# Optimization experiments

Measured on AMD Instinct MI355X. Metric: run time of the kernel, lower is better.

The kernel has to match this reference:

```python
import jax, jax.numpy as jnp
import numpy as np

B, T, D, U, R = 64, 512, 256, 256, 4


def setup_inputs() -> dict:
    key = jax.random.key(0)
    ks = jax.random.split(key, 12)
    inputs = jax.random.normal(ks[0], (B, T, D), dtype=jnp.float32)
    # per-timestep dependency indices into past timesteps; must satisfy dep[t] <= t
    dependencies = jnp.minimum(
        jax.random.randint(ks[1], (T, R - 1), 0, T), jnp.arange(T)[:, None]
    ).astype(jnp.int32)
    mask = jax.random.randint(ks[2], (B, T), 0, 2).astype(jnp.int32)
    initial_states = jax.random.normal(ks[3], (R, B, U), dtype=jnp.float32) * 0.1
    s = 1.0 / np.sqrt(U)
    def w(k, shape):
        return jax.random.normal(k, shape, dtype=jnp.float32) * s
    return dict(
        inputs=inputs, dependencies=dependencies, mask=mask, initial_states=initial_states,
        Wz=w(ks[4], (D, U)), Wr=w(ks[5], (D, U)), Wh=w(ks[6], (D, U)),
        Uz=w(ks[7], (U, U)), Ur=w(ks[8], (U, U)), Uh=w(ks[9], (U, U)),
        bz=jnp.zeros((U,), jnp.float32), br=jnp.zeros((U,), jnp.float32), bh=jnp.zeros((U,), jnp.float32),
    )


def reference(inputs, dependencies, mask, initial_states, Wz, Wr, Wh, Uz, Ur, Uh, bz, br, bh):
    Bn, Tn, _ = inputs.shape
    Rn = initial_states.shape[0]
    Un = Uz.shape[0]

    x = jnp.swapaxes(inputs, 0, 1)              # [T, B, D]  (time_major swap)
    m = jnp.swapaxes(mask, 0, 1).astype(bool)   # [T, B]
    # dependencies[i] is consumed AFTER step i (sets states for step i+1) -> shift by one
    dep_in = jnp.concatenate(
        [jnp.zeros((1, dependencies.shape[1]), dependencies.dtype), dependencies[:-1]], axis=0
    )

    def cell(x_t, states):
        # states: [R, B, U]  (child-sum Graph-GRU over recurrent_size predecessor states)
        r = jax.nn.sigmoid(x_t @ Wr + states @ Ur + br)          # [R, B, U]
        h_sum = states.sum(0)                                    # [B, U]
        z = jax.nn.sigmoid(x_t @ Wz + h_sum @ Uz + bz)
        h_tilde = jnp.tanh(x_t @ Wh + (r * states).sum(0) @ Uh + bh)
        h = z * (h_sum / Rn) + (1.0 - z) * h_tilde
        return h  # GRU: output == new state

    def step(carry, xs):
        prev_out, prev_state, buf, t = carry
        x_t, m_t, dep_t = xs
        gathered = buf[dep_t]                                    # [R-1, B, U] irregular history gather
        cand = jnp.concatenate([prev_state[None], gathered], axis=0)
        states = jnp.where(t == 0, initial_states, cand)
        h = cell(x_t, states)
        mt = m_t[:, None]                                        # [B, 1]
        out_m = jnp.where(mt, h, prev_out)                       # masked output (pre_output carry)
        st_m = jnp.where(mt, h, prev_state)                      # masked state  (pre_states carry)
        buf = buf.at[t].set(st_m)                                # successive_states[t]
        return (out_m, st_m, buf, t + 1), out_m

    carry0 = (
        jnp.zeros((Bn, Un), inputs.dtype),
        jnp.zeros((Bn, Un), inputs.dtype),
        jnp.zeros((Tn, Bn, Un), inputs.dtype),
        jnp.array(0, jnp.int32),
    )
    (last_out, last_state, _, _), outs = jax.lax.scan(step, carry0, (x, m, dep_in))

    # zero_output_for_mask
    last_out = jnp.where(m[-1][:, None], last_out, jnp.zeros_like(last_out))
    outs = jnp.where(m[:, :, None], outs, jnp.zeros_like(outs))
    outputs = jnp.swapaxes(outs, 0, 1)                           # back to [B, T, U]
    return outputs, last_out, last_state
```

## Files before the change

### kernel.cpp

```cpp
#include <hip/hip_runtime.h>
#include <cstdint>
#include <cstddef>

#define BN 64
#define TN 512
#define DN 256
#define UN 256
#define NC 768
#define SLOTS (TN + 5)
#define ZSLOT (TN + 4)

__device__ __forceinline__ float sigm(float x) {
  return 1.0f / (1.0f + __expf(-x));
}
__device__ __forceinline__ float tanh_fast(float x) {
  float e = __expf(-2.0f * x);
  return 2.0f / (1.0f + e) - 1.0f;
}

__global__ __launch_bounds__(256) void build_wcat(
    const float* __restrict__ Wr, const float* __restrict__ Wz, const float* __restrict__ Wh,
    const float* __restrict__ br, const float* __restrict__ bz, const float* __restrict__ bh,
    float* __restrict__ wcat, float* __restrict__ bias)
{
  int idx = blockIdx.x * 256 + threadIdx.x;
  if (idx < DN * NC) {
    int k = idx / NC, c = idx % NC;
    float v;
    if (c < 256)      v = Wr[k * UN + c];
    else if (c < 512) v = Wz[k * UN + (c - 256)];
    else              v = Wh[k * UN + (c - 512)];
    wcat[idx] = v;
  }
  if (idx < NC) {
    bias[idx] = (idx < 256) ? br[idx] : ((idx < 512) ? bz[idx - 256] : bh[idx - 512]);
  }
}

__global__ __launch_bounds__(256) void gemm_xw(
    const float* __restrict__ X, const float* __restrict__ Wc,
    const float* __restrict__ bias, float* __restrict__ P)
{
  __shared__ float As[32][68];
  __shared__ float Bs[32][64];
  const int tid = threadIdx.x;
  const int m0 = blockIdx.x * 64;
  const int n0 = blockIdx.y * 64;
  const int ty = tid >> 4, tx = tid & 15;
  float acc[4][4] = {};

  const int ar = tid >> 3;
  const int ak = (tid & 7) * 4;
  const int bk = tid >> 4;
  const int bn = (tid & 15) * 4;

  for (int k0 = 0; k0 < DN; k0 += 32) {
    float4 a0 = *(const float4*)(X + (size_t)(m0 + ar) * DN + k0 + ak);
    float4 a1 = *(const float4*)(X + (size_t)(m0 + 32 + ar) * DN + k0 + ak);
    As[ak + 0][ar] = a0.x; As[ak + 1][ar] = a0.y; As[ak + 2][ar] = a0.z; As[ak + 3][ar] = a0.w;
    As[ak + 0][32 + ar] = a1.x; As[ak + 1][32 + ar] = a1.y; As[ak + 2][32 + ar] = a1.z; As[ak + 3][32 + ar] = a1.w;
    *(float4*)&Bs[bk][bn]      = *(const float4*)(Wc + (size_t)(k0 + bk) * NC + n0 + bn);
    *(float4*)&Bs[bk + 16][bn] = *(const float4*)(Wc + (size_t)(k0 + bk + 16) * NC + n0 + bn);
    __syncthreads();
#pragma unroll
    for (int kk = 0; kk < 32; kk++) {
      float4 av = *(const float4*)&As[kk][ty * 4];
      float4 bv = *(const float4*)&Bs[kk][tx * 4];
      acc[0][0] += av.x * bv.x; acc[0][1] += av.x * bv.y; acc[0][2] += av.x * bv.z; acc[0][3] += av.x * bv.w;
      acc[1][0] += av.y * bv.x; acc[1][1] += av.y * bv.y; acc[1][2] += av.y * bv.z; acc[1][3] += av.y * bv.w;
      acc[2][0] += av.z * bv.x; acc[2][1] += av.z * bv.y; acc[2][2] += av.z * bv.z; acc[2][3] += av.z * bv.w;
      acc[3][0] += av.w * bv.x; acc[3][1] += av.w * bv.y; acc[3][2] += av.w * bv.z; acc[3][3] += av.w * bv.w;
    }
    __syncthreads();
  }
  float4 bb = *(const float4*)(bias + n0 + tx * 4);
#pragma unroll
  for (int i = 0; i < 4; i++) {
    float4 o;
    o.x = acc[i][0] + bb.x; o.y = acc[i][1] + bb.y;
    o.z = acc[i][2] + bb.z; o.w = acc[i][3] + bb.w;
    *(float4*)(P + (size_t)(m0 + ty * 4 + i) * NC + n0 + tx * 4) = o;
  }
}

__global__ __launch_bounds__(1024, 4) void recurrent_kernel(
    const float* __restrict__ P,
    const float* __restrict__ Ur, const float* __restrict__ Uz, const float* __restrict__ Uh,
    const int* __restrict__ dep, const int* __restrict__ mask,
    const float* __restrict__ init,
    float* __restrict__ out,
    float* __restrict__ buf_s, float* __restrict__ buf_pr, float* __restrict__ buf_pz)
{
  const int b = blockIdx.x;
  const int tid = threadIdx.x;
  const int g = tid >> 8;
  const int u = tid & 255;
  const int qd = tid >> 6;
  const int cd = (tid & 63) * 4;

  float wh[64];
  {
    const float* p2 = Uh + (size_t)(64 * g) * UN + u;
#pragma unroll
    for (int kk = 0; kk < 64; kk++) {
      wh[kk] = p2[(size_t)kk * UN];
    }
  }

  __shared__ float ls[4][256], lpr[4][256], lpz[4][256];
  __shared__ float lx[NC];
  __shared__ float rs[256], hs[256], zv[256], hv[256];
  __shared__ float red0[4][256];
  __shared__ float reddR[16][256], reddZ[16][256];
  __shared__ float scur[256], prcur[256], pzcur[256];
  __shared__ int eff[TN];
  __shared__ int mloc[TN];
  __shared__ int deploc[TN * 3];

  for (int i = tid; i < TN; i += 1024) mloc[i] = mask[b * TN + i];
  for (int i = tid; i < TN * 3; i += 1024) deploc[i] = dep[i];

  const size_t bufBase = (size_t)b * SLOTS * UN;

  {
    float v = init[((size_t)g * BN + b) * UN + u];
    ls[g][u] = v;
    buf_s[bufBase + (size_t)(TN + g) * UN + u] = v;
    if (tid < 256) {
      scur[u] = 0.0f; prcur[u] = 0.0f; pzcur[u] = 0.0f;
      buf_s[bufBase + (size_t)ZSLOT * UN + u] = 0.0f;
      buf_pr[bufBase + (size_t)ZSLOT * UN + u] = 0.0f;
      buf_pz[bufBase + (size_t)ZSLOT * UN + u] = 0.0f;
    }
  }
  __syncthreads();

#pragma unroll 1
  for (int gg = 0; gg < 4; gg++) {
    float4 arA = {0, 0, 0, 0}, azA = {0, 0, 0, 0};
    const float* bR = Ur + (size_t)(qd * 16) * UN + cd;
    const float* bZ = Uz + (size_t)(qd * 16) * UN + cd;
#pragma unroll 4
    for (int kk = 0; kk < 16; kk++) {
      float hk = ls[gg][qd * 16 + kk];
      float4 w1 = *(const float4*)(bR + (size_t)kk * UN);
      float4 w2 = *(const float4*)(bZ + (size_t)kk * UN);
      arA.x = fmaf(hk, w1.x, arA.x); arA.y = fmaf(hk, w1.y, arA.y);
      arA.z = fmaf(hk, w1.z, arA.z); arA.w = fmaf(hk, w1.w, arA.w);
      azA.x = fmaf(hk, w2.x, azA.x); azA.y = fmaf(hk, w2.y, azA.y);
      azA.z = fmaf(hk, w2.z, azA.z); azA.w = fmaf(hk, w2.w, azA.w);
    }
    *(float4*)&reddR[qd][cd] = arA;
    *(float4*)&reddZ[qd][cd] = azA;
    __syncthreads();
    if (tid < 256) {
      float prn = 0.0f, pzn = 0.0f;
#pragma unroll
      for (int q = 0; q < 16; q++) { prn += reddR[q][tid]; pzn += reddZ[q][tid]; }
      buf_pr[bufBase + (size_t)(TN + gg) * UN + tid] = prn;
      buf_pz[bufBase + (size_t)(TN + gg) * UN + tid] = pzn;
    }
    __syncthreads();
  }

  const size_t outB = (size_t)b * TN * UN;
  const size_t pB = (size_t)b * TN * NC;

#pragma unroll 1
  for (int t = 0; t < TN; t++) {
    const int m = mloc[t];
    if (m == 0) {
      if (tid < 256) out[outB + (size_t)t * UN + u] = 0.0f;
      if (tid == 0) eff[t] = (t == 0) ? ZSLOT : eff[t - 1];
      __syncthreads();
      continue;
    }
    if (t > 0 && g == 0) {
      ls[0][u] = scur[u]; lpr[0][u] = prcur[u]; lpz[0][u] = pzcur[u];
    } else {
      int src = (t == 0) ? (TN + g) : eff[deploc[(t - 1) * 3 + (g - 1)]];
      size_t base = bufBase + (size_t)src * UN + u;
      ls[g][u]  = buf_s[base];
      lpr[g][u] = buf_pr[base];
      lpz[g][u] = buf_pz[base];
    }
    if (tid < NC) lx[tid] = P[pB + (size_t)t * NC + tid];
    __syncthreads();
    if (tid < 256) {
      float s0 = ls[0][u], s1 = ls[1][u], s2 = ls[2][u], s3 = ls[3][u];
      float xr = lx[u];
      float r0 = sigm(xr + lpr[0][u]);
      float r1 = sigm(xr + lpr[1][u]);
      float r2 = sigm(xr + lpr[2][u]);
      float r3 = sigm(xr + lpr[3][u]);
      rs[u] = r0 * s0 + r1 * s1 + r2 * s2 + r3 * s3;
      hs[u] = (s0 + s1) + (s2 + s3);
      zv[u] = sigm(lx[256 + u] + ((lpz[0][u] + lpz[1][u]) + (lpz[2][u] + lpz[3][u])));
    }
    __syncthreads();
    {
      float a0 = 0, a1 = 0, a2 = 0, a3 = 0;
      const float4* v4 = (const float4*)&rs[64 * g];
#pragma unroll
      for (int kk = 0; kk < 16; kk++) {
        float4 v = v4[kk];
        a0 += v.x * wh[4 * kk];     a1 += v.y * wh[4 * kk + 1];
        a2 += v.z * wh[4 * kk + 2]; a3 += v.w * wh[4 * kk + 3];
      }
      red0[g][u] = (a0 + a1) + (a2 + a3);
    }
    __syncthreads();
    if (tid < 256) {
      float ht = tanh_fast(lx[512 + u] + ((red0[0][u] + red0[1][u]) + (red0[2][u] + red0[3][u])));
      float z = zv[u];
      float h = z * hs[u] * 0.25f + (1.0f - z) * ht;
      hv[u] = h; scur[u] = h;
      out[outB + (size_t)t * UN + u] = h;
    }
    __syncthreads();
    {
      float4 arA = {0, 0, 0, 0}, azA = {0, 0, 0, 0};
      const float* bR = Ur + (size_t)(qd * 16) * UN + cd;
      const float* bZ = Uz + (size_t)(qd * 16) * UN + cd;
#pragma unroll 4
      for (int kk = 0; kk < 16; kk++) {
        float hk = hv[qd * 16 + kk];
        float4 w1 = *(const float4*)(bR + (size_t)kk * UN);
        float4 w2 = *(const float4*)(bZ + (size_t)kk * UN);
        arA.x = fmaf(hk, w1.x, arA.x); arA.y = fmaf(hk, w1.y, arA.y);
        arA.z = fmaf(hk, w1.z, arA.z); arA.w = fmaf(hk, w1.w, arA.w);
        azA.x = fmaf(hk, w2.x, azA.x); azA.y = fmaf(hk, w2.y, azA.y);
        azA.z = fmaf(hk, w2.z, azA.z); azA.w = fmaf(hk, w2.w, azA.w);
      }
      *(float4*)&reddR[qd][cd] = arA;
      *(float4*)&reddZ[qd][cd] = azA;
    }
    __syncthreads();
    if (tid < 256) {
      float prn = 0.0f, pzn = 0.0f;
#pragma unroll
      for (int q = 0; q < 16; q++) { prn += reddR[q][tid]; pzn += reddZ[q][tid]; }
      prcur[tid] = prn; pzcur[tid] = pzn;
      size_t base = bufBase + (size_t)t * UN + tid;
      buf_s[base]  = hv[tid];
      buf_pr[base] = prn;
      buf_pz[base] = pzn;
    }
    if (tid == 0) eff[t] = t;
    __syncthreads();
  }

  if (tid < 256) {
    float lst = scur[u];
    out[(size_t)BN * TN * UN + (size_t)b * UN + u] = mloc[TN - 1] ? lst : 0.0f;
    out[(size_t)BN * TN * UN + (size_t)BN * UN + (size_t)b * UN + u] = lst;
  }
}

extern "C" void kernel_launch(void* const* d_in, const int* in_sizes, int n_in,
                              void* d_out, int out_size, void* d_ws, size_t ws_size,
                              hipStream_t stream) {
  const float* inputs       = (const float*)d_in[0];
  const int*   dependencies = (const int*)d_in[1];
  const int*   mask         = (const int*)d_in[2];
  const float* initial      = (const float*)d_in[3];
  const float* Wz = (const float*)d_in[4];
  const float* Wr = (const float*)d_in[5];
  const float* Wh = (const float*)d_in[6];
  const float* Uz = (const float*)d_in[7];
  const float* Ur = (const float*)d_in[8];
  const float* Uh = (const float*)d_in[9];
  const float* bz = (const float*)d_in[10];
  const float* br = (const float*)d_in[11];
  const float* bh = (const float*)d_in[12];

  float* out = (float*)d_out;
  float* ws  = (float*)d_ws;
  float* wcat    = ws;
  float* bias    = wcat + (size_t)DN * NC;
  float* precomp = bias + NC;
  float* buf_s   = precomp + (size_t)BN * TN * NC;
  float* buf_pr  = buf_s + (size_t)BN * SLOTS * UN;
  float* buf_pz  = buf_pr + (size_t)BN * SLOTS * UN;

  build_wcat<<<(DN * NC + 255) / 256, 256, 0, stream>>>(Wr, Wz, Wh, br, bz, bh, wcat, bias);
  gemm_xw<<<dim3(BN * TN / 64, NC / 64), 256, 0, stream>>>(inputs, wcat, bias, precomp);
  recurrent_kernel<<<BN, 1024, 0, stream>>>(precomp, Ur, Uz, Uh, dependencies, mask, initial,
                                            out, buf_s, buf_pr, buf_pz);
}
```

Baseline: 2.062 ms.

## Cache leading rows of Ur/Uz in LDS and split projection by matrix

Restructures the per-step Ur/Uz projection so each wave handles a single matrix over a 32-row k-slice, instead of both matrices over a 16-row slice. The first WL=6 rows of each slice are preloaded into shared memory and the remaining rows still stream from global/L2. The partial-sum reduction drops from 16 to 8 terms per output. This cuts global weight traffic on the serial critical path, at the cost of about 96KB more LDS per block and a longer per-wave k-loop.

After: 1.870 ms. 1.1x faster.

```diff
diff --git a/kernel.cpp b/kernel.cpp
--- a/kernel.cpp
+++ b/kernel.cpp
@@ -9,6 +9,7 @@
 #define NC 768
 #define SLOTS (TN + 5)
 #define ZSLOT (TN + 4)
+#define WL 6
 
 __device__ __forceinline__ float sigm(float x) {
   return 1.0f / (1.0f + __expf(-x));
@@ -95,8 +96,10 @@
   const int tid = threadIdx.x;
   const int g = tid >> 8;
   const int u = tid & 255;
-  const int qd = tid >> 6;
-  const int cd = (tid & 63) * 4;
+  const int wv = tid >> 6;
+  const int mat = wv & 1;
+  const int s   = wv >> 1;
+  const int l   = tid & 63;
 
   float wh[64];
   {
@@ -106,17 +109,27 @@
       wh[kk] = p2[(size_t)kk * UN];
     }
   }
-
+  const float* Um = mat ? Uz : Ur;
+
+  __shared__ float4 wlds[2][8][WL][64];
   __shared__ float ls[4][256], lpr[4][256], lpz[4][256];
   __shared__ float lx[NC];
   __shared__ float rs[256], hs[256], zv[256], hv[256];
   __shared__ float red0[4][256];
-  __shared__ float reddR[16][256], reddZ[16][256];
+  __shared__ float redd[2][8][256];
   __shared__ float scur[256], prcur[256], pzcur[256];
   __shared__ int eff[TN];
   __shared__ int mloc[TN];
   __shared__ int deploc[TN * 3];
 
+  for (int i = tid; i < 2 * 8 * WL * 64; i += 1024) {
+    int mm = i / (8 * WL * 64);
+    int r2 = i % (8 * WL * 64);
+    int ss = r2 / (WL * 64);
+    int rr = (r2 / 64) % WL;
+    int ll = i & 63;
+    wlds[mm][ss][rr][ll] = ((const float4*)(mm ? Uz : Ur))[(size_t)(32 * ss + rr) * 64 + ll];
+  }
   for (int i = tid; i < TN; i += 1024) mloc[i] = mask[b * TN + i];
   for (int i = tid; i < TN * 3; i += 1024) deploc[i] = dep[i];
 
@@ -135,28 +148,35 @@
   }
   __syncthreads();
 
+  auto projD = [&](const float* hsrc) {
+    const float* hb = hsrc + 32 * s;
+    float4 a = {0, 0, 0, 0};
+#pragma unroll
+    for (int r = 0; r < WL; r++) {
+      float hk = hb[r];
+      float4 w = wlds[mat][s][r][l];
+      a.x = fmaf(hk, w.x, a.x); a.y = fmaf(hk, w.y, a.y);
+      a.z = fmaf(hk, w.z, a.z); a.w = fmaf(hk, w.w, a.w);
+    }
+    const float4* p = (const float4*)Um + (size_t)(32 * s + WL) * 64 + l;
+#pragma unroll 4
+    for (int r = 0; r < 32 - WL; r++) {
+      float hk = hb[WL + r];
+      float4 w = p[(size_t)r * 64];
+      a.x = fmaf(hk, w.x, a.x); a.y = fmaf(hk, w.y, a.y);
+      a.z = fmaf(hk, w.z, a.z); a.w = fmaf(hk, w.w, a.w);
+    }
+    *(float4*)&redd[mat][s][4 * l] = a;
+  };
+
 #pragma unroll 1
   for (int gg = 0; gg < 4; gg++) {
-    float4 arA = {0, 0, 0, 0}, azA = {0, 0, 0, 0};
-    const float* bR = Ur + (size_t)(qd * 16) * UN + cd;
-    const float* bZ = Uz + (size_t)(qd * 16) * UN + cd;
-#pragma unroll 4
-    for (int kk = 0; kk < 16; kk++) {
-      float hk = ls[gg][qd * 16 + kk];
-      float4 w1 = *(const float4*)(bR + (size_t)kk * UN);
-      float4 w2 = *(const float4*)(bZ + (size_t)kk * UN);
-      arA.x = fmaf(hk, w1.x, arA.x); arA.y = fmaf(hk, w1.y, arA.y);
-      arA.z = fmaf(hk, w1.z, arA.z); arA.w = fmaf(hk, w1.w, arA.w);
-      azA.x = fmaf(hk, w2.x, azA.x); azA.y = fmaf(hk, w2.y, azA.y);
-      azA.z = fmaf(hk, w2.z, azA.z); azA.w = fmaf(hk, w2.w, azA.w);
-    }
-    *(float4*)&reddR[qd][cd] = arA;
-    *(float4*)&reddZ[qd][cd] = azA;
+    projD(&ls[gg][0]);
     __syncthreads();
     if (tid < 256) {
       float prn = 0.0f, pzn = 0.0f;
 #pragma unroll
-      for (int q = 0; q < 16; q++) { prn += reddR[q][tid]; pzn += reddZ[q][tid]; }
+      for (int q = 0; q < 8; q++) { prn += redd[0][q][tid]; pzn += redd[1][q][tid]; }
       buf_pr[bufBase + (size_t)(TN + gg) * UN + tid] = prn;
       buf_pz[bufBase + (size_t)(TN + gg) * UN + tid] = pzn;
     }
@@ -218,28 +238,12 @@
       out[outB + (size_t)t * UN + u] = h;
     }
     __syncthreads();
-    {
-      float4 arA = {0, 0, 0, 0}, azA = {0, 0, 0, 0};
-      const float* bR = Ur + (size_t)(qd * 16) * UN + cd;
-      const float* bZ = Uz + (size_t)(qd * 16) * UN + cd;
-#pragma unroll 4
-      for (int kk = 0; kk < 16; kk++) {
-        float hk = hv[qd * 16 + kk];
-        float4 w1 = *(const float4*)(bR + (size_t)kk * UN);
-        float4 w2 = *(const float4*)(bZ + (size_t)kk * UN);
-        arA.x = fmaf(hk, w1.x, arA.x); arA.y = fmaf(hk, w1.y, arA.y);
-        arA.z = fmaf(hk, w1.z, arA.z); arA.w = fmaf(hk, w1.w, arA.w);
-        azA.x = fmaf(hk, w2.x, azA.x); azA.y = fmaf(hk, w2.y, azA.y);
-        azA.z = fmaf(hk, w2.z, azA.z); azA.w = fmaf(hk, w2.w, azA.w);
-      }
-      *(float4*)&reddR[qd][cd] = arA;
-      *(float4*)&reddZ[qd][cd] = azA;
-    }
+    projD(hv);
     __syncthreads();
     if (tid < 256) {
       float prn = 0.0f, pzn = 0.0f;
 #pragma unroll
-      for (int q = 0; q < 16; q++) { prn += reddR[q][tid]; pzn += reddZ[q][tid]; }
+      for (int q = 0; q < 8; q++) { prn += redd[0][q][tid]; pzn += redd[1][q][tid]; }
       prcur[tid] = prn; pzcur[tid] = pzn;
       size_t base = bufBase + (size_t)t * UN + tid;
       buf_s[base]  = hv[tid];
```
